# Optimization experiments

Hardware: AMD Instinct MI355X
Metric: run time of the kernel (lower is better)

Reference implementation:

```python
import jax, jax.numpy as jnp
import numpy as np

ALPHA = 50.0
BETA = 0.5
EPS = 1e-6

def setup_inputs() -> dict:
    key = jax.random.key(0)
    k1, k2, k3 = jax.random.split(key, 3)
    N, D = 131072, 512
    output1 = jax.random.normal(k1, (N, D), dtype=jnp.float32)
    output2 = jax.random.normal(k2, (N, D), dtype=jnp.float32)
    target = jax.random.randint(k3, (N,), 0, 2, dtype=jnp.int64)
    return {"output1": output1, "output2": output2, "target": target}

def reference(output1, output2, target):
    # per-pair cosine similarity (torch.nn.CosineSimilarity, dim=1, eps=1e-6)
    dot = jnp.sum(output1 * output2, axis=1)
    denom = jnp.maximum(jnp.linalg.norm(output1, axis=1) * jnp.linalg.norm(output2, axis=1), EPS)
    d = dot / denom  # [N]
    # binomial deviance terms
    pos = (2.0 / BETA) * jax.nn.softplus(-BETA * (d - 0.5))
    neg = (2.0 / ALPHA) * jax.nn.softplus(ALPHA * (d - 2.0))
    is_pos = (target == 1)
    num_pos = jnp.sum(is_pos)
    num_neg = target.shape[0] - num_pos
    pos_loss = jnp.sum(jnp.where(is_pos, pos, 0.0)) / jnp.maximum(num_pos, 1)
    neg_loss = jnp.sum(jnp.where(is_pos, 0.0, neg)) / jnp.maximum(num_neg, 1)
    return pos_loss + neg_loss
```

## Files before the change

kernel.cpp:

```cpp
#include <hip/hip_runtime.h>
#include <math.h>

#define N_ROWS 131072
#define D 512
#define BLOCKS 2048
#define WPB 4
#define NWAVES (BLOCKS * WPB)
#define ROWS_PER_WAVE (N_ROWS / NWAVES)
#define N_IT (ROWS_PER_WAVE / 2)
#define EPS 1e-6f

__device__ __forceinline__ float softplusf(float x) {
    return fmaxf(x, 0.0f) + log1pf(__expf(-fabsf(x)));
}

struct Frag {
    float4 a[4];
    float4 b[4];
};

__device__ __forceinline__ void issue_loads(const float* __restrict__ o1,
                                            const float* __restrict__ o2,
                                            size_t elem, Frag& f) {
    const float* p1 = o1 + elem;
    const float* p2 = o2 + elem;
    #pragma unroll
    for (int j = 0; j < 4; ++j) {
        f.a[j] = *(const float4*)(p1 + j * 128);
        f.b[j] = *(const float4*)(p2 + j * 128);
    }
}

__device__ __forceinline__ void process(const Frag& f, int t0, int t1, int rl, int sub,
                                        float& posAcc, float& negAcc, int& posCnt) {
    float dot = 0.0f, s1 = 0.0f, s2 = 0.0f;
    #pragma unroll
    for (int j = 0; j < 4; ++j) {
        float4 a = f.a[j];
        float4 v = f.b[j];
        dot += a.x * v.x + a.y * v.y + a.z * v.z + a.w * v.w;
        s1  += a.x * a.x + a.y * a.y + a.z * a.z + a.w * a.w;
        s2  += v.x * v.x + v.y * v.y + v.z * v.z + v.w * v.w;
    }
    #pragma unroll
    for (int off = 16; off > 0; off >>= 1) {
        dot += __shfl_xor(dot, off);
        s1  += __shfl_xor(s1, off);
        s2  += __shfl_xor(s2, off);
    }
    if (sub == 0) {
        float d = dot / fmaxf(sqrtf(s1) * sqrtf(s2), EPS);
        int t = rl ? t1 : t0;
        if (t == 1) { posAcc += 4.0f * softplusf(-0.5f * (d - 0.5f)); posCnt++; }
        else        { negAcc += 0.04f * softplusf(50.0f * (d - 2.0f)); }
    }
}

__global__ __launch_bounds__(256, 4) void binloss_main(
    const float* __restrict__ o1, const float* __restrict__ o2,
    const int* __restrict__ target,
    float* __restrict__ sums, int* __restrict__ icnt,
    unsigned int* __restrict__ done, float* __restrict__ out) {

    __shared__ float sPos[WPB], sNeg[WPB];
    __shared__ int sCnt[WPB];

    const int lane = threadIdx.x & 63;
    const int wave = threadIdx.x >> 6;
    const int gwave = blockIdx.x * WPB + wave;
    const int rowBase = gwave * ROWS_PER_WAVE;
    const int sub = lane & 31;
    const int rl = lane >> 5;

    const int myT = target[rowBase + (lane & (ROWS_PER_WAVE - 1))];

    const size_t colOff = (size_t)sub * 4;

    float posAcc = 0.0f, negAcc = 0.0f;
    int posCnt = 0;

    Frag fA, fB;
    issue_loads(o1, o2, (size_t)(rowBase + rl) * D + colOff, fA);

    for (int k = 0; k < N_IT; k += 2) {
        issue_loads(o1, o2, (size_t)(rowBase + 2 * (k + 1) + rl) * D + colOff, fB);

        process(fA, __shfl(myT, 2 * k), __shfl(myT, 2 * k + 1), rl, sub,
                posAcc, negAcc, posCnt);

        if (k + 2 < N_IT)
            issue_loads(o1, o2, (size_t)(rowBase + 2 * (k + 2) + rl) * D + colOff, fA);

        process(fB, __shfl(myT, 2 * k + 2), __shfl(myT, 2 * k + 3), rl, sub,
                posAcc, negAcc, posCnt);
    }

    posAcc += __shfl_xor(posAcc, 32);
    negAcc += __shfl_xor(negAcc, 32);
    posCnt += __shfl_xor(posCnt, 32);

    if (lane == 0) { sPos[wave] = posAcc; sNeg[wave] = negAcc; sCnt[wave] = posCnt; }
    __syncthreads();
    if (threadIdx.x == 0) {
        float p = sPos[0] + sPos[1] + sPos[2] + sPos[3];
        float n = sNeg[0] + sNeg[1] + sNeg[2] + sNeg[3];
        int c = sCnt[0] + sCnt[1] + sCnt[2] + sCnt[3];
        atomicAdd(&sums[0], p);
        atomicAdd(&sums[1], n);
        atomicAdd(&icnt[0], c);
        __threadfence();
        unsigned int old = atomicAdd(done, 1u);
        if (old == (unsigned int)(gridDim.x - 1)) {
            __threadfence();
            float ps = __hip_atomic_load(&sums[0], __ATOMIC_RELAXED, __HIP_MEMORY_SCOPE_AGENT);
            float ns = __hip_atomic_load(&sums[1], __ATOMIC_RELAXED, __HIP_MEMORY_SCOPE_AGENT);
            int np = __hip_atomic_load(&icnt[0], __ATOMIC_RELAXED, __HIP_MEMORY_SCOPE_AGENT);
            int nn = N_ROWS - np;
            out[0] = ps / (float)(np > 1 ? np : 1) + ns / (float)(nn > 1 ? nn : 1);
        }
    }
}

extern "C" void kernel_launch(void* const* d_in, const int* in_sizes, int n_in,
                              void* d_out, int out_size, void* d_ws, size_t ws_size,
                              hipStream_t stream) {
    const float* o1 = (const float*)d_in[0];
    const float* o2 = (const float*)d_in[1];
    const int* tgt = (const int*)d_in[2];
    float* out = (float*)d_out;
    float* sums = (float*)d_ws;
    int* cnt = (int*)((char*)d_ws + 8);
    unsigned int* done = (unsigned int*)((char*)d_ws + 12);

    hipMemsetAsync(d_ws, 0, 16, stream);
    binloss_main<<<BLOCKS, 256, 0, stream>>>(o1, o2, tgt, sums, cnt, done, out);
}
```

Baseline: 588.9 us.

## Process one row per wave with 4-deep pipelined loads and deferred loss

Each wave now handles one full row per step (64 lanes × 8 floats) instead of two half-wave rows. Loads go through a 4-slot software pipeline controlled by explicit s_waitcnt vmcnt values and sched barriers, so three rows of loads stay in flight while one row is reduced. The per-row dot/norms are stashed in the owning lane, and softplus plus target selection run once per lane at the end instead of on a single lane inside the loop. The cost is more registers for four slots, a longer 6-step shuffle reduction per row, and reliance on hand-coded waitcnt encoding and a fully unrolled count of 16 rows per wave.

Result: slower. 604.6 us (+2.7%).

```diff
diff --git a/kernel.cpp b/kernel.cpp
--- a/kernel.cpp
+++ b/kernel.cpp
@@ -6,55 +6,48 @@
 #define BLOCKS 2048
 #define WPB 4
 #define NWAVES (BLOCKS * WPB)
-#define ROWS_PER_WAVE (N_ROWS / NWAVES)
-#define N_IT (ROWS_PER_WAVE / 2)
+#define RPW (N_ROWS / NWAVES)
 #define EPS 1e-6f
+
+#define WAIT_VM(N) __builtin_amdgcn_s_waitcnt(0x0F70 | ((N) & 0xF) | ((((N) >> 4) & 3) << 14))
+#define PIN() __builtin_amdgcn_sched_barrier(0)
 
 __device__ __forceinline__ float softplusf(float x) {
     return fmaxf(x, 0.0f) + log1pf(__expf(-fabsf(x)));
 }
 
-struct Frag {
-    float4 a[4];
-    float4 b[4];
-};
+struct Slot { float4 a0, a1, b0, b1; };
 
-__device__ __forceinline__ void issue_loads(const float* __restrict__ o1,
-                                            const float* __restrict__ o2,
-                                            size_t elem, Frag& f) {
-    const float* p1 = o1 + elem;
-    const float* p2 = o2 + elem;
+#define ISSUE(S, T) do {                                        \
+    const float* _p1 = pRow1 + (size_t)(T) * D;                 \
+    const float* _p2 = pRow2 + (size_t)(T) * D;                 \
+    S.a0 = *(const float4*)(_p1);                               \
+    S.a1 = *(const float4*)(_p1 + 256);                         \
+    S.b0 = *(const float4*)(_p2);                               \
+    S.b1 = *(const float4*)(_p2 + 256);                         \
+} while (0)
+
+__device__ __forceinline__ void proc_tile(const Slot& s, int t, int lane,
+                                          float& myDot, float& myS1, float& myS2) {
+    float dot = s.a0.x * s.b0.x + s.a0.y * s.b0.y + s.a0.z * s.b0.z + s.a0.w * s.b0.w
+              + s.a1.x * s.b1.x + s.a1.y * s.b1.y + s.a1.z * s.b1.z + s.a1.w * s.b1.w;
+    float s1  = s.a0.x * s.a0.x + s.a0.y * s.a0.y + s.a0.z * s.a0.z + s.a0.w * s.a0.w
+              + s.a1.x * s.a1.x + s.a1.y * s.a1.y + s.a1.z * s.a1.z + s.a1.w * s.a1.w;
+    float s2  = s.b0.x * s.b0.x + s.b0.y * s.b0.y + s.b0.z * s.b0.z + s.b0.w * s.b0.w
+              + s.b1.x * s.b1.x + s.b1.y * s.b1.y + s.b1.z * s.b1.z + s.b1.w * s.b1.w;
     #pragma unroll
-    for (int j = 0; j < 4; ++j) {
-        f.a[j] = *(const float4*)(p1 + j * 128);
-        f.b[j] = *(const float4*)(p2 + j * 128);
-    }
-}
-
-__device__ __forceinline__ void process(const Frag& f, int t0, int t1, int rl, int sub,
-                                        float& posAcc, float& negAcc, int& posCnt) {
-    float dot = 0.0f, s1 = 0.0f, s2 = 0.0f;
-    #pragma unroll
-    for (int j = 0; j < 4; ++j) {
-        float4 a = f.a[j];
-        float4 v = f.b[j];
-        dot += a.x * v.x + a.y * v.y + a.z * v.z + a.w * v.w;
-        s1  += a.x * a.x + a.y * a.y + a.z * a.z + a.w * a.w;
-        s2  += v.x * v.x + v.y * v.y + v.z * v.z + v.w * v.w;
-    }
-    #pragma unroll
-    for (int off = 16; off > 0; off >>= 1) {
+    for (int off = 32; off > 0; off >>= 1) {
         dot += __shfl_xor(dot, off);
         s1  += __shfl_xor(s1, off);
         s2  += __shfl_xor(s2, off);
     }
-    if (sub == 0) {
-        float d = dot / fmaxf(sqrtf(s1) * sqrtf(s2), EPS);
-        int t = rl ? t1 : t0;
-        if (t == 1) { posAcc += 4.0f * softplusf(-0.5f * (d - 0.5f)); posCnt++; }
-        else        { negAcc += 0.04f * softplusf(50.0f * (d - 2.0f)); }
-    }
+    if (lane == t) { myDot = dot; myS1 = s1; myS2 = s2; }
 }
+
+#define STEP(SI, TI, SP, TP) do {                                \
+    ISSUE(SI, TI); PIN(); WAIT_VM(12); PIN();                    \
+    proc_tile(SP, TP, lane, myDot, myS1, myS2);                  \
+} while (0)
 
 __global__ __launch_bounds__(256, 4) void binloss_main(
     const float* __restrict__ o1, const float* __restrict__ o2,
@@ -68,38 +61,54 @@
     const int lane = threadIdx.x & 63;
     const int wave = threadIdx.x >> 6;
     const int gwave = blockIdx.x * WPB + wave;
-    const int rowBase = gwave * ROWS_PER_WAVE;
-    const int sub = lane & 31;
-    const int rl = lane >> 5;
+    const int rowBase = gwave * RPW;
 
-    const int myT = target[rowBase + (lane & (ROWS_PER_WAVE - 1))];
+    const int myT = target[rowBase + (lane & (RPW - 1))];
 
-    const size_t colOff = (size_t)sub * 4;
+    const float* pRow1 = o1 + (size_t)rowBase * D + lane * 4;
+    const float* pRow2 = o2 + (size_t)rowBase * D + lane * 4;
 
-    float posAcc = 0.0f, negAcc = 0.0f;
-    int posCnt = 0;
+    float myDot = 0.0f, myS1 = 1.0f, myS2 = 1.0f;
 
-    Frag fA, fB;
-    issue_loads(o1, o2, (size_t)(rowBase + rl) * D + colOff, fA);
+    Slot s0, s1_, s2_, s3;
 
-    for (int k = 0; k < N_IT; k += 2) {
-        issue_loads(o1, o2, (size_t)(rowBase + 2 * (k + 1) + rl) * D + colOff, fB);
+    ISSUE(s0, 0);
+    ISSUE(s1_, 1);
+    ISSUE(s2_, 2);
 
-        process(fA, __shfl(myT, 2 * k), __shfl(myT, 2 * k + 1), rl, sub,
-                posAcc, negAcc, posCnt);
+    STEP(s3, 3,  s0, 0);
+    STEP(s0, 4,  s1_, 1);
+    STEP(s1_, 5, s2_, 2);
+    STEP(s2_, 6, s3, 3);
+    STEP(s3, 7,  s0, 4);
+    STEP(s0, 8,  s1_, 5);
+    STEP(s1_, 9, s2_, 6);
+    STEP(s2_, 10, s3, 7);
+    STEP(s3, 11, s0, 8);
+    STEP(s0, 12, s1_, 9);
+    STEP(s1_, 13, s2_, 10);
+    STEP(s2_, 14, s3, 11);
+    STEP(s3, 15, s0, 12);
+    WAIT_VM(8);  PIN(); proc_tile(s1_, 13, lane, myDot, myS1, myS2);
+    WAIT_VM(4);  PIN(); proc_tile(s2_, 14, lane, myDot, myS1, myS2);
+    WAIT_VM(0);  PIN(); proc_tile(s3, 15, lane, myDot, myS1, myS2);
 
-        if (k + 2 < N_IT)
-            issue_loads(o1, o2, (size_t)(rowBase + 2 * (k + 2) + rl) * D + colOff, fA);
-
-        process(fB, __shfl(myT, 2 * k + 2), __shfl(myT, 2 * k + 3), rl, sub,
-                posAcc, negAcc, posCnt);
+    float d = myDot / fmaxf(sqrtf(myS1) * sqrtf(myS2), EPS);
+    float posv = 0.0f, negv = 0.0f;
+    int pc = 0;
+    if (lane < RPW) {
+        if (myT == 1) { posv = 4.0f * softplusf(-0.5f * (d - 0.5f)); pc = 1; }
+        else          { negv = 0.04f * softplusf(50.0f * (d - 2.0f)); }
     }
 
-    posAcc += __shfl_xor(posAcc, 32);
-    negAcc += __shfl_xor(negAcc, 32);
-    posCnt += __shfl_xor(posCnt, 32);
+    #pragma unroll
+    for (int off = 32; off > 0; off >>= 1) {
+        posv += __shfl_xor(posv, off);
+        negv += __shfl_xor(negv, off);
+        pc   += __shfl_xor(pc, off);
+    }
 
-    if (lane == 0) { sPos[wave] = posAcc; sNeg[wave] = negAcc; sCnt[wave] = posCnt; }
+    if (lane == 0) { sPos[wave] = posv; sNeg[wave] = negv; sCnt[wave] = pc; }
     __syncthreads();
     if (threadIdx.x == 0) {
         float p = sPos[0] + sPos[1] + sPos[2] + sPos[3];
```
